# Performance work log

Measured on AMD Instinct MI355X. Metric: run time of the kernel, lower is better.

The kernel has to match this reference:

```python
import jax, jax.numpy as jnp
import numpy as np

TOP_K = 2


def setup_inputs() -> dict:
    key = jax.random.key(0)
    ks = jax.random.split(key, 6)
    B, S, H, I, E = 4, 2048, 1024, 4096, 8
    x = jax.random.normal(ks[0], (B, S, H), dtype=jnp.float32)
    Wr = jax.random.normal(ks[1], (H, E), dtype=jnp.float32) * (1.0 / np.sqrt(H))
    W1 = jax.random.normal(ks[2], (E, H, I), dtype=jnp.float32) * (1.0 / np.sqrt(H))
    b1 = jnp.zeros((E, I), dtype=jnp.float32)
    W2 = jax.random.normal(ks[3], (E, I, H), dtype=jnp.float32) * (1.0 / np.sqrt(I))
    b2 = jnp.zeros((E, H), dtype=jnp.float32)
    return {"x": x, "Wr": Wr, "W1": W1, "b1": b1, "W2": W2, "b2": b2}


def reference(x, Wr, W1, b1, W2, b2):
    B, S, H = x.shape
    E = Wr.shape[1]
    xf = x.reshape(-1, H)                              # [T, H], T = B*S
    logits = xf @ Wr                                   # [T, E]
    probs = jax.nn.softmax(logits, axis=-1)
    rw, sel = jax.lax.top_k(probs, TOP_K)              # [T, K]
    rw = rw / jnp.sum(rw, axis=-1, keepdims=True)
    out = jnp.zeros_like(xf)
    # Loop over small fixed expert count; each token contributes only via its
    # top-k combine weight (zero weight == not routed, matching index_add).
    for i in range(E):
        wi = jnp.sum(jnp.where(sel == i, rw, 0.0), axis=-1)    # [T]
        h = jax.nn.silu(xf @ W1[i] + b1[i])                    # [T, I]
        out = out + (h @ W2[i] + b2[i]) * wi[:, None]
    return out.reshape(B, S, H)
```

## Files before the change

kernel.cpp:

```cpp
#include <hip/hip_runtime.h>
#include <cstdint>
#include <cstddef>

#define TTOK 8192
#define HDIM 1024
#define IDIM 4096
#define NEXP 8
#define PMAX 18432
#define WS_NEED 302260352ULL

#define SLOT1 24576
#define SLOT2 16384

typedef __attribute__((ext_vector_type(8))) short bf16x8;
typedef __attribute__((ext_vector_type(4))) float f32x4;

#define AS3 __attribute__((address_space(3)))
#define AS1 __attribute__((address_space(1)))

__device__ __forceinline__ void gld16(const void* g, void* s) {
  __builtin_amdgcn_global_load_lds((const AS1 void*)g, (AS3 void*)s, 16, 0, 0);
}

__device__ __forceinline__ void pinned_barrier() {
  __builtin_amdgcn_sched_barrier(0);
  __builtin_amdgcn_s_barrier();
  __builtin_amdgcn_sched_barrier(0);
}

__device__ __forceinline__ unsigned short f2b(float f) {
  unsigned u = __builtin_bit_cast(unsigned, f);
  unsigned r = ((u >> 16) & 1u) + 0x7FFFu;
  return (unsigned short)((u + r) >> 16);
}

__device__ __forceinline__ float b2f(unsigned short u) {
  return __builtin_bit_cast(float, ((unsigned)u) << 16);
}


__device__ __forceinline__ void router_body(
    int bid, int t, const float* __restrict__ x, const float* __restrict__ wr,
    unsigned short* __restrict__ xb, int* __restrict__ t2e,
    float* __restrict__ t2w)
{
  const int tok = bid * 4 + (t >> 6);
  const int l = t & 63;
  const float* xr = x + (size_t)tok * HDIM;
  float acc[8] = {0.f,0.f,0.f,0.f,0.f,0.f,0.f,0.f};
  #pragma unroll
  for (int j = 0; j < 4; ++j) {
    const int base = j * 256 + l * 4;
    const float4 xv = *(const float4*)(xr + base);
    const float xa[4] = {xv.x, xv.y, xv.z, xv.w};
    ushort4 ub;
    ub.x = f2b(xa[0]); ub.y = f2b(xa[1]); ub.z = f2b(xa[2]); ub.w = f2b(xa[3]);
    *(ushort4*)(xb + (size_t)tok * HDIM + base) = ub;
    #pragma unroll
    for (int ii = 0; ii < 4; ++ii) {
      const float4 w0 = *(const float4*)(wr + (size_t)(base + ii) * 8);
      const float4 w1 = *(const float4*)(wr + (size_t)(base + ii) * 8 + 4);
      acc[0] += xa[ii] * w0.x; acc[1] += xa[ii] * w0.y;
      acc[2] += xa[ii] * w0.z; acc[3] += xa[ii] * w0.w;
      acc[4] += xa[ii] * w1.x; acc[5] += xa[ii] * w1.y;
      acc[6] += xa[ii] * w1.z; acc[7] += xa[ii] * w1.w;
    }
  }
  #pragma unroll
  for (int e = 0; e < 8; ++e) {
    float v = acc[e];
    #pragma unroll
    for (int off = 32; off > 0; off >>= 1) v += __shfl_xor(v, off);
    acc[e] = v;
  }
  if (l == 0) {
    float l0 = -1e30f; int i0 = 0;
    #pragma unroll
    for (int e = 0; e < 8; ++e) if (acc[e] > l0) { l0 = acc[e]; i0 = e; }
    float l1 = -1e30f; int i1 = (i0 == 0) ? 1 : 0;
    #pragma unroll
    for (int e = 0; e < 8; ++e) if (e != i0 && acc[e] > l1) { l1 = acc[e]; i1 = e; }
    const float w0 = 1.f / (1.f + expf(l1 - l0));
    t2e[tok * 2] = i0; t2e[tok * 2 + 1] = i1;
    t2w[tok * 2] = w0; t2w[tok * 2 + 1] = 1.f - w0;
  }
}

__device__ __forceinline__ void packT_body(
    int bid, int t, uint32_t* __restrict__ plds,
    const float* __restrict__ src, unsigned short* __restrict__ dst,
    int K, int N)
{
  const int tiles_n = N >> 8, tiles_k = K >> 5;
  const int e = bid / (tiles_k * tiles_n);
  const int rem = bid % (tiles_k * tiles_n);
  const int kt = rem / tiles_n, it = rem % tiles_n;
  const float* S = src + (size_t)e * K * N + (size_t)kt * 32 * N + (size_t)it * 256;
  unsigned short* D = dst + (size_t)e * N * K + (size_t)it * 256 * K + (size_t)kt * 32;
  #pragma unroll
  for (int q = 0; q < 4; ++q) {
    const int task = q * 256 + t;
    const int i4 = task & 63, kp = task >> 6;
    const float* p0 = S + (size_t)(2 * kp) * N + i4 * 4;
    const float4 r0 = *(const float4*)p0;
    const float4 r1 = *(const float4*)(p0 + N);
    const float a0[4] = {r0.x, r0.y, r0.z, r0.w};
    const float a1[4] = {r1.x, r1.y, r1.z, r1.w};
    #pragma unroll
    for (int j = 0; j < 4; ++j)
      plds[(i4 * 4 + j) * 17 + kp] = (uint32_t)f2b(a0[j]) | ((uint32_t)f2b(a1[j]) << 16);
  }
  __syncthreads();
  #pragma unroll
  for (int r = 0; r < 4; ++r) {
    const int idx = r * 256 + t;
    const int il = idx >> 2, q4 = idx & 3;
    uint4 o;
    o.x = plds[il * 17 + q4 * 4 + 0];
    o.y = plds[il * 17 + q4 * 4 + 1];
    o.z = plds[il * 17 + q4 * 4 + 2];
    o.w = plds[il * 17 + q4 * 4 + 3];
    *(uint4*)(D + (size_t)il * K + q4 * 8) = o;
  }
}

__global__ __launch_bounds__(256, 2) void prep_k(
    const float* __restrict__ x, const float* __restrict__ wr,
    unsigned short* __restrict__ xb, int* __restrict__ t2e,
    float* __restrict__ t2w,
    const float* __restrict__ w1, unsigned short* __restrict__ w1t,
    const float* __restrict__ w2, unsigned short* __restrict__ w2t)
{
  __shared__ uint32_t plds[256 * 17];
  const int bid = blockIdx.x, t = threadIdx.x;
  if (bid < 2048) {
    router_body(bid, t, x, wr, xb, t2e, t2w);
  } else if (bid < 2048 + 4096) {
    packT_body(bid - 2048, t, plds, w1, w1t, HDIM, IDIM);
  } else {
    packT_body(bid - 6144, t, plds, w2, w2t, IDIM, HDIM);
  }
}

__global__ void scatter_k(const int* __restrict__ t2e, int* __restrict__ meta,
                          int* __restrict__ ltok, int* __restrict__ t2p)
{
  const int e = blockIdx.x;
  const int t = threadIdx.x, w = t >> 6, l = t & 63;
  __shared__ int part[4][8];
  __shared__ int soff, scnt;
  {
    int cnt[8] = {0,0,0,0,0,0,0,0};
    for (int c = 0; c < 32; ++c) {
      const int tok = (w * 32 + c) * 64 + l;
      const int e0 = t2e[2 * tok], e1 = t2e[2 * tok + 1];
      #pragma unroll
      for (int i = 0; i < 8; ++i)
        cnt[i] += __popcll(__ballot(e0 == i)) + __popcll(__ballot(e1 == i));
    }
    if (l == 0) {
      #pragma unroll
      for (int i = 0; i < 8; ++i) part[w][i] = cnt[i];
    }
  }
  __syncthreads();
  if (t == 0) {
    int off = 0, mycnt = 0, tot = 0;
    #pragma unroll
    for (int i = 0; i < 8; ++i) {
      const int s = part[0][i] + part[1][i] + part[2][i] + part[3][i];
      const int pad = (s + 255) & ~255;
      if (i == e) mycnt = s;
      if (i < e) off += pad;
      tot += pad;
    }
    soff = off; scnt = mycnt;
    meta[16 + e] = off;
    if (e == 0) meta[24] = tot;
  }
  __syncthreads();
  const int off = soff, cnt = scnt;

  __shared__ int wsum[4];
  __shared__ int base;
  if (t == 0) base = 0;
  __syncthreads();
  const unsigned long long lt = (1ULL << l) - 1ULL;
  for (int c = 0; c < TTOK / 256; ++c) {
    const int tok = c * 256 + t;
    const bool m0 = (t2e[2 * tok] == e);
    const bool m1 = (t2e[2 * tok + 1] == e);
    const unsigned long long b0 = __ballot(m0);
    const unsigned long long b1 = __ballot(m1);
    const int n0 = __popcll(b0), n1 = __popcll(b1);
    const int r0 = __popcll(b0 & lt);
    const int r1 = n0 + __popcll(b1 & lt);
    if (l == 0) wsum[w] = n0 + n1;
    __syncthreads();
    int wb = base;
    #pragma unroll
    for (int i = 0; i < 4; ++i) if (i < w) wb += wsum[i];
    const int tot = wsum[0] + wsum[1] + wsum[2] + wsum[3];
    __syncthreads();
    if (t == 0) base += tot;
    if (m0) { const int p = off + wb + r0; ltok[p] = tok; t2p[2 * tok] = p; }
    if (m1) { const int p = off + wb + r1; ltok[p] = tok; t2p[2 * tok + 1] = p; }
    __syncthreads();
  }
  const int padded = (cnt + 255) & ~255;
  for (int i = cnt + t; i < padded; i += 256) ltok[off + i] = -1;
}


__global__ __launch_bounds__(512, 4) void gemm1_k(
    const unsigned short* __restrict__ xb, const unsigned short* __restrict__ w1t,
    const float* __restrict__ b1, const int* __restrict__ meta,
    const int* __restrict__ ltok, unsigned short* __restrict__ h)
{
  const int wg = blockIdx.x;
  const int id = (wg & 7) * (2304 / 8) + (wg >> 3);
  const int mt = id >> 5, nt = id & 31;
  if (mt * 256 >= meta[24]) return;
  int e = 0;
  #pragma unroll
  for (int i = 1; i < 8; ++i) if (meta[16 + i] <= mt * 256) e = i;

  extern __shared__ char lds[];
  const int t = threadIdx.x;
  const int w = t >> 6, l = t & 63;
  const int wn = w & 1, wm = w >> 1;

  const unsigned short* asrc;
  {
    const int G = t;
    const int line = G >> 3, q = (G & 7) ^ (line & 7);
    const int row = 2 * line + (q >> 2), g = q & 3;
    asrc = w1t + ((size_t)e * IDIM + nt * 128 + row) * HDIM + g * 8;
  }
  const unsigned short* bsrc[2];
  #pragma unroll
  for (int c = 0; c < 2; ++c) {
    const int G = c * 512 + t;
    const int line = G >> 3, q = (G & 7) ^ (line & 7);
    const int row = 2 * line + (q >> 2), g = q & 3;
    int tok = ltok[mt * 256 + row]; if (tok < 0) tok = 0;
    bsrc[c] = xb + (size_t)tok * HDIM + g * 8;
  }

  const int lr = l & 15, lg = l >> 4;
  f32x4 acc[4][4] = {};

  auto STAGE = [&](int kt) {
    char* sb = lds + (kt % 3) * SLOT1;
    const int ks = kt * 32;
    gld16(asrc + ks, sb + w * 1024);
    gld16(bsrc[0] + ks, sb + 8192 + w * 1024);
    gld16(bsrc[1] + ks, sb + 16384 + w * 1024);
  };

  STAGE(0); STAGE(1);
  const int NT = HDIM / 32;
  for (int kt = 0; kt < NT; ++kt) {
    if (kt + 1 < NT) {
      asm volatile("s_waitcnt vmcnt(3)" ::: "memory");
    } else {
      asm volatile("s_waitcnt vmcnt(0)" ::: "memory");
    }
    pinned_barrier();
    const char* sl = lds + (kt % 3) * SLOT1;
    bf16x8 af[4], bf[4];
    #pragma unroll
    for (int f = 0; f < 4; ++f) {
      const int rowA = wn * 64 + f * 16 + lr;
      const int lineA = rowA >> 1;
      const int pA = (((rowA & 1) << 2) + lg) ^ (lineA & 7);
      af[f] = *(const bf16x8*)(sl + lineA * 128 + pA * 16);
      const int rowB = wm * 64 + f * 16 + lr;
      const int lineB = rowB >> 1;
      const int pB = (((rowB & 1) << 2) + lg) ^ (lineB & 7);
      bf[f] = *(const bf16x8*)(sl + 8192 + lineB * 128 + pB * 16);
    }
    if (kt + 2 < NT) STAGE(kt + 2);
    __builtin_amdgcn_s_setprio(1);
    #pragma unroll
    for (int fm = 0; fm < 4; ++fm)
      #pragma unroll
      for (int fn = 0; fn < 4; ++fn)
        acc[fm][fn] = __builtin_amdgcn_mfma_f32_16x16x32_bf16(af[fm], bf[fn], acc[fm][fn], 0, 0, 0);
    __builtin_amdgcn_s_setprio(0);
    pinned_barrier();
  }

  const int lg4 = lg * 4;
  #pragma unroll
  for (int fm = 0; fm < 4; ++fm) {
    const int ib = nt * 128 + wn * 64 + fm * 16 + lg4;
    const float4 b1v = *(const float4*)(b1 + e * IDIM + ib);
    #pragma unroll
    for (int fn = 0; fn < 4; ++fn) {
      const int trow = mt * 256 + wm * 64 + fn * 16 + lr;
      const float v0 = acc[fm][fn][0] + b1v.x;
      const float v1 = acc[fm][fn][1] + b1v.y;
      const float v2 = acc[fm][fn][2] + b1v.z;
      const float v3 = acc[fm][fn][3] + b1v.w;
      ushort4 st;
      st.x = f2b(v0 / (1.f + __expf(-v0)));
      st.y = f2b(v1 / (1.f + __expf(-v1)));
      st.z = f2b(v2 / (1.f + __expf(-v2)));
      st.w = f2b(v3 / (1.f + __expf(-v3)));
      *(ushort4*)(h + (size_t)trow * IDIM + ib) = st;
    }
  }
}

__global__ __launch_bounds__(256, 3) void gemm2_k(
    const unsigned short* __restrict__ h, const unsigned short* __restrict__ w2t,
    const int* __restrict__ meta, unsigned short* __restrict__ y)
{
  const int wg = blockIdx.x;
  const int id = (wg & 7) * (2304 / 8) + (wg >> 3);
  const int nt = id & 7, kh = (id >> 3) & 1, mt = id >> 4;
  if (mt * 128 >= meta[24]) return;
  int e = 0;
  #pragma unroll
  for (int i = 1; i < 8; ++i) if (meta[16 + i] <= mt * 128) e = i;

  extern __shared__ char lds[];
  const int t = threadIdx.x;
  const int w = t >> 6, l = t & 63;
  const int wn = w & 1, wm = w >> 1;
  const int kbase = kh * (IDIM / 2);

  const unsigned short* asrc[2]; const unsigned short* bsrc[2];
  #pragma unroll
  for (int c = 0; c < 2; ++c) {
    const int G = c * 256 + t;
    const int line = G >> 3, q = (G & 7) ^ (line & 7);
    const int row = 2 * line + (q >> 2), g = q & 3;
    asrc[c] = w2t + ((size_t)e * HDIM + nt * 128 + row) * IDIM + kbase + g * 8;
    bsrc[c] = h + (size_t)(mt * 128 + row) * IDIM + kbase + g * 8;
  }

  const int lr = l & 15, lg = l >> 4;
  f32x4 acc[4][4] = {};

  auto STAGE = [&](int kt) {
    char* sb = lds + (kt % 3) * SLOT2;
    const int ks = kt * 32;
    gld16(asrc[0] + ks, sb + w * 1024);
    gld16(asrc[1] + ks, sb + 4096 + w * 1024);
    gld16(bsrc[0] + ks, sb + 8192 + w * 1024);
    gld16(bsrc[1] + ks, sb + 12288 + w * 1024);
  };

  STAGE(0); STAGE(1);
  const int NT = IDIM / 2 / 32;
  for (int kt = 0; kt < NT; ++kt) {
    if (kt + 1 < NT) {
      asm volatile("s_waitcnt vmcnt(4)" ::: "memory");
    } else {
      asm volatile("s_waitcnt vmcnt(0)" ::: "memory");
    }
    pinned_barrier();
    const char* sl = lds + (kt % 3) * SLOT2;
    bf16x8 af[4], bf[4];
    #pragma unroll
    for (int f = 0; f < 4; ++f) {
      const int rowA = wn * 64 + f * 16 + lr;
      const int lineA = rowA >> 1;
      const int pA = (((rowA & 1) << 2) + lg) ^ (lineA & 7);
      af[f] = *(const bf16x8*)(sl + lineA * 128 + pA * 16);
      const int rowB = wm * 64 + f * 16 + lr;
      const int lineB = rowB >> 1;
      const int pB = (((rowB & 1) << 2) + lg) ^ (lineB & 7);
      bf[f] = *(const bf16x8*)(sl + 8192 + lineB * 128 + pB * 16);
    }
    if (kt + 2 < NT) STAGE(kt + 2);
    __builtin_amdgcn_s_setprio(1);
    #pragma unroll
    for (int fm = 0; fm < 4; ++fm)
      #pragma unroll
      for (int fn = 0; fn < 4; ++fn)
        acc[fm][fn] = __builtin_amdgcn_mfma_f32_16x16x32_bf16(af[fm], bf[fn], acc[fm][fn], 0, 0, 0);
    __builtin_amdgcn_s_setprio(0);
    pinned_barrier();
  }

  unsigned short* yo = y + (size_t)kh * PMAX * HDIM;
  const int lg4 = lg * 4;
  #pragma unroll
  for (int fm = 0; fm < 4; ++fm) {
    const int colb = nt * 128 + wn * 64 + fm * 16 + lg4;
    #pragma unroll
    for (int fn = 0; fn < 4; ++fn) {
      const int row = mt * 128 + wm * 64 + fn * 16 + lr;
      ushort4 st;
      st.x = f2b(acc[fm][fn][0]); st.y = f2b(acc[fm][fn][1]);
      st.z = f2b(acc[fm][fn][2]); st.w = f2b(acc[fm][fn][3]);
      *(ushort4*)(yo + (size_t)row * HDIM + colb) = st;
    }
  }
}

__global__ __launch_bounds__(256, 4) void combine_k(
    const unsigned short* __restrict__ y, const float* __restrict__ b2,
    const int* __restrict__ t2e, const float* __restrict__ t2w,
    const int* __restrict__ t2p, float* __restrict__ out)
{
  const int t = blockIdx.x * 4 + (threadIdx.x >> 6);
  const int l = threadIdx.x & 63;
  const int e0 = t2e[t * 2], e1 = t2e[t * 2 + 1];
  const float w0 = t2w[t * 2], w1v = t2w[t * 2 + 1];
  const int p0 = t2p[t * 2], p1 = t2p[t * 2 + 1];
  const unsigned short* ya0 = y + (size_t)p0 * HDIM;
  const unsigned short* yb0 = y + (size_t)PMAX * HDIM + (size_t)p0 * HDIM;
  const unsigned short* ya1 = y + (size_t)p1 * HDIM;
  const unsigned short* yb1 = y + (size_t)PMAX * HDIM + (size_t)p1 * HDIM;
  const float* bb0 = b2 + e0 * HDIM;
  const float* bb1 = b2 + e1 * HDIM;
  float* o = out + (size_t)t * HDIM;
  #pragma unroll
  for (int j = 0; j < 4; ++j) {
    const int c = j * 256 + l * 4;
    const ushort4 a0 = *(const ushort4*)(ya0 + c);
    const ushort4 a1 = *(const ushort4*)(yb0 + c);
    const ushort4 b0v = *(const ushort4*)(ya1 + c);
    const ushort4 b1u = *(const ushort4*)(yb1 + c);
    const float4 c0 = *(const float4*)(bb0 + c);
    const float4 c1 = *(const float4*)(bb1 + c);
    float4 r;
    r.x = w0 * (b2f(a0.x) + b2f(a1.x) + c0.x) + w1v * (b2f(b0v.x) + b2f(b1u.x) + c1.x);
    r.y = w0 * (b2f(a0.y) + b2f(a1.y) + c0.y) + w1v * (b2f(b0v.y) + b2f(b1u.y) + c1.y);
    r.z = w0 * (b2f(a0.z) + b2f(a1.z) + c0.z) + w1v * (b2f(b0v.z) + b2f(b1u.z) + c1.z);
    r.w = w0 * (b2f(a0.w) + b2f(a1.w) + c0.w) + w1v * (b2f(b0v.w) + b2f(b1u.w) + c1.w);
    *(float4*)(o + c) = r;
  }
}

__global__ void sentinel_k(float* out) { out[0] = 1.0e6f; }

extern "C" void kernel_launch(void* const* d_in, const int* in_sizes, int n_in,
                              void* d_out, int out_size, void* d_ws, size_t ws_size,
                              hipStream_t stream)
{
  (void)in_sizes; (void)n_in; (void)out_size;
  const float* x  = (const float*)d_in[0];
  const float* wr = (const float*)d_in[1];
  const float* w1 = (const float*)d_in[2];
  const float* b1 = (const float*)d_in[3];
  const float* w2 = (const float*)d_in[4];
  const float* b2 = (const float*)d_in[5];
  float* out = (float*)d_out;
  char* ws = (char*)d_ws;

  if (ws_size < WS_NEED) { sentinel_k<<<1, 1, 0, stream>>>(out); return; }

  unsigned short* xb  = (unsigned short*)(ws);
  unsigned short* w1t = (unsigned short*)(ws + 16777216);
  unsigned short* w2t = (unsigned short*)(ws + 83886080);
  unsigned short* h   = (unsigned short*)(ws + 150994944);
  int*   t2e  = (int*)(ws + 301989888);
  float* t2w  = (float*)(ws + 302055424);
  int*   ltok = (int*)(ws + 302120960);
  int*   t2p  = (int*)(ws + 302194688);
  int*   meta = (int*)(ws + 302260224);
  unsigned short* y = (unsigned short*)(ws);

  hipFuncSetAttribute((const void*)gemm1_k, hipFuncAttributeMaxDynamicSharedMemorySize, 3 * SLOT1);
  hipFuncSetAttribute((const void*)gemm2_k, hipFuncAttributeMaxDynamicSharedMemorySize, 3 * SLOT2);

  prep_k<<<10240, 256, 0, stream>>>(x, wr, xb, t2e, t2w, w1, w1t, w2, w2t);
  scatter_k<<<NEXP, 256, 0, stream>>>(t2e, meta, ltok, t2p);

  gemm1_k<<<72 * 32, 512, 3 * SLOT1, stream>>>(xb, w1t, b1, meta, ltok, h);
  gemm2_k<<<144 * 8 * 2, 256, 3 * SLOT2, stream>>>(h, w2t, meta, y);
  combine_k<<<TTOK / 4, 256, 0, stream>>>(y, b2, t2e, t2w, t2p, out);
}
```

Before: 536.0 us.

## Enlarge gemm1 tile to 256x256 with 64-wide K and phased ping-pong pipeline

The first expert GEMM now uses 256x256 output tiles per workgroup, with each wave computing a 128x64 sub-tile over K steps of 64, and double-buffers 128KB of LDS. Global-to-LDS loads are split into quarter-stages interleaved with MFMA phases. This raises data reuse per byte loaded and cuts the number of workgroups. In exchange, occupancy drops to 2 blocks per CU with higher register pressure, and there are more barriers per iteration.

```diff
diff --git a/kernel.cpp b/kernel.cpp
--- a/kernel.cpp
+++ b/kernel.cpp
@@ -9,7 +9,6 @@
 #define PMAX 18432
 #define WS_NEED 302260352ULL
 
-#define SLOT1 24576
 #define SLOT2 16384
 
 typedef __attribute__((ext_vector_type(8))) short bf16x8;
@@ -25,6 +24,11 @@
 __device__ __forceinline__ void pinned_barrier() {
   __builtin_amdgcn_sched_barrier(0);
   __builtin_amdgcn_s_barrier();
+  __builtin_amdgcn_sched_barrier(0);
+}
+
+__device__ __forceinline__ void wait_lds() {
+  asm volatile("s_waitcnt lgkmcnt(0)" ::: "memory");
   __builtin_amdgcn_sched_barrier(0);
 }
 
@@ -211,15 +215,14 @@
   for (int i = cnt + t; i < padded; i += 256) ltok[off + i] = -1;
 }
 
-
-__global__ __launch_bounds__(512, 4) void gemm1_k(
+__global__ __launch_bounds__(512, 2) void gemm1_k(
     const unsigned short* __restrict__ xb, const unsigned short* __restrict__ w1t,
     const float* __restrict__ b1, const int* __restrict__ meta,
     const int* __restrict__ ltok, unsigned short* __restrict__ h)
 {
   const int wg = blockIdx.x;
-  const int id = (wg & 7) * (2304 / 8) + (wg >> 3);
-  const int mt = id >> 5, nt = id & 31;
+  const int id = (wg & 7) * (1152 / 8) + (wg >> 3);
+  const int mt = id >> 4, nt = id & 15;
   if (mt * 256 >= meta[24]) return;
   int e = 0;
   #pragma unroll
@@ -228,77 +231,226 @@
   extern __shared__ char lds[];
   const int t = threadIdx.x;
   const int w = t >> 6, l = t & 63;
-  const int wn = w & 1, wm = w >> 1;
-
-  const unsigned short* asrc;
-  {
-    const int G = t;
-    const int line = G >> 3, q = (G & 7) ^ (line & 7);
-    const int row = 2 * line + (q >> 2), g = q & 3;
-    asrc = w1t + ((size_t)e * IDIM + nt * 128 + row) * HDIM + g * 8;
-  }
-  const unsigned short* bsrc[2];
-  #pragma unroll
-  for (int c = 0; c < 2; ++c) {
-    const int G = c * 512 + t;
-    const int line = G >> 3, q = (G & 7) ^ (line & 7);
-    const int row = 2 * line + (q >> 2), g = q & 3;
-    int tok = ltok[mt * 256 + row]; if (tok < 0) tok = 0;
-    bsrc[c] = xb + (size_t)tok * HDIM + g * 8;
-  }
-
+  const int wm = w >> 2, wn = w & 3;
   const int lr = l & 15, lg = l >> 4;
-  f32x4 acc[4][4] = {};
-
-  auto STAGE = [&](int kt) {
-    char* sb = lds + (kt % 3) * SLOT1;
-    const int ks = kt * 32;
-    gld16(asrc + ks, sb + w * 1024);
-    gld16(bsrc[0] + ks, sb + 8192 + w * 1024);
-    gld16(bsrc[1] + ks, sb + 16384 + w * 1024);
+
+  const int srow = t >> 3;
+  const int sg = (t & 7) ^ (srow & 7);
+  const unsigned short* asrc[2][2];
+  const unsigned short* bsrc[2][2];
+  #pragma unroll
+  for (int hh = 0; hh < 2; ++hh)
+    #pragma unroll
+    for (int s = 0; s < 2; ++s) {
+      const int row = hh * 128 + s * 64 + srow;
+      asrc[hh][s] = w1t + ((size_t)e * IDIM + nt * 256 + row) * HDIM + sg * 8;
+      int tok = ltok[mt * 256 + row]; if (tok < 0) tok = 0;
+      bsrc[hh][s] = xb + (size_t)tok * HDIM + sg * 8;
+    }
+
+  auto STG = [&](int kt, int o, int hh) {
+    char* d = lds + (kt & 1) * 65536 + o * 32768 + hh * 16384 + w * 1024;
+    const int ks = kt * 64;
+    const unsigned short* s0 = o ? bsrc[hh][0] : asrc[hh][0];
+    const unsigned short* s1 = o ? bsrc[hh][1] : asrc[hh][1];
+    gld16(s0 + ks, d);
+    gld16(s1 + ks, d + 8192);
   };
 
-  STAGE(0); STAGE(1);
-  const int NT = HDIM / 32;
-  for (int kt = 0; kt < NT; ++kt) {
-    if (kt + 1 < NT) {
-      asm volatile("s_waitcnt vmcnt(3)" ::: "memory");
-    } else {
-      asm volatile("s_waitcnt vmcnt(0)" ::: "memory");
-    }
-    pinned_barrier();
-    const char* sl = lds + (kt % 3) * SLOT1;
-    bf16x8 af[4], bf[4];
-    #pragma unroll
-    for (int f = 0; f < 4; ++f) {
-      const int rowA = wn * 64 + f * 16 + lr;
-      const int lineA = rowA >> 1;
-      const int pA = (((rowA & 1) << 2) + lg) ^ (lineA & 7);
-      af[f] = *(const bf16x8*)(sl + lineA * 128 + pA * 16);
-      const int rowB = wm * 64 + f * 16 + lr;
-      const int lineB = rowB >> 1;
-      const int pB = (((rowB & 1) << 2) + lg) ^ (lineB & 7);
-      bf[f] = *(const bf16x8*)(sl + 8192 + lineB * 128 + pB * 16);
-    }
-    if (kt + 2 < NT) STAGE(kt + 2);
-    __builtin_amdgcn_s_setprio(1);
-    #pragma unroll
-    for (int fm = 0; fm < 4; ++fm)
-      #pragma unroll
-      for (int fn = 0; fn < 4; ++fn)
-        acc[fm][fn] = __builtin_amdgcn_mfma_f32_16x16x32_bf16(af[fm], bf[fn], acc[fm][fn], 0, 0, 0);
+  f32x4 acc[8][4] = {};
+  const int NITER = (HDIM / 64) / 2;
+
+  STG(0, 1, 0); STG(0, 1, 1);
+  STG(0, 0, 0); STG(0, 0, 1);
+  STG(1, 1, 0); STG(1, 1, 1);
+  asm volatile("s_waitcnt vmcnt(4)" ::: "memory");
+  pinned_barrier();
+
+  for (int it = 0; it < NITER; ++it) {
+    const int t1 = 2 * it + 1, t2 = 2 * it + 2, t3 = 2 * it + 3;
+    const bool pf = (it + 1 < NITER);
+    const char* sA0 = lds + wm * 16384;
+    const char* sB0 = lds + 32768 + (wn >> 1) * 16384;
+    const char* sA1 = sA0 + 65536;
+    const char* sB1 = sB0 + 65536;
+    const int rB = (wn & 1) * 64;
+
+    bf16x8 af[4][2], b01[2][2], b23[2][2];
+
+    #pragma unroll
+    for (int fm = 0; fm < 4; ++fm)
+      #pragma unroll
+      for (int ks = 0; ks < 2; ++ks) {
+        const int row = fm * 16 + lr;
+        af[fm][ks] = *(const bf16x8*)(sA0 + row * 128 + (((ks << 2) + lg) ^ (row & 7)) * 16);
+      }
+    #pragma unroll
+    for (int fn = 0; fn < 2; ++fn)
+      #pragma unroll
+      for (int ks = 0; ks < 2; ++ks) {
+        const int row = rB + fn * 16 + lr;
+        b01[fn][ks] = *(const bf16x8*)(sB0 + row * 128 + (((ks << 2) + lg) ^ (row & 7)) * 16);
+      }
+    STG(t1, 0, 0);
+    pinned_barrier(); wait_lds();
+    __builtin_amdgcn_s_setprio(1);
+    #pragma unroll
+    for (int fm = 0; fm < 4; ++fm)
+      #pragma unroll
+      for (int fn = 0; fn < 2; ++fn) {
+        acc[fm][fn] = __builtin_amdgcn_mfma_f32_16x16x32_bf16(af[fm][0], b01[fn][0], acc[fm][fn], 0, 0, 0);
+        acc[fm][fn] = __builtin_amdgcn_mfma_f32_16x16x32_bf16(af[fm][1], b01[fn][1], acc[fm][fn], 0, 0, 0);
+      }
+    __builtin_amdgcn_s_setprio(0);
+    pinned_barrier();
+
+    #pragma unroll
+    for (int fn = 0; fn < 2; ++fn)
+      #pragma unroll
+      for (int ks = 0; ks < 2; ++ks) {
+        const int row = rB + (fn + 2) * 16 + lr;
+        b23[fn][ks] = *(const bf16x8*)(sB0 + row * 128 + (((ks << 2) + lg) ^ (row & 7)) * 16);
+      }
+    STG(t1, 0, 1);
+    pinned_barrier(); wait_lds();
+    __builtin_amdgcn_s_setprio(1);
+    #pragma unroll
+    for (int fm = 0; fm < 4; ++fm)
+      #pragma unroll
+      for (int fn = 0; fn < 2; ++fn) {
+        acc[fm][fn + 2] = __builtin_amdgcn_mfma_f32_16x16x32_bf16(af[fm][0], b23[fn][0], acc[fm][fn + 2], 0, 0, 0);
+        acc[fm][fn + 2] = __builtin_amdgcn_mfma_f32_16x16x32_bf16(af[fm][1], b23[fn][1], acc[fm][fn + 2], 0, 0, 0);
+      }
+    __builtin_amdgcn_s_setprio(0);
+    pinned_barrier();
+
+    #pragma unroll
+    for (int fm = 0; fm < 4; ++fm)
+      #pragma unroll
+      for (int ks = 0; ks < 2; ++ks) {
+        const int row = (fm + 4) * 16 + lr;
+        af[fm][ks] = *(const bf16x8*)(sA0 + row * 128 + (((ks << 2) + lg) ^ (row & 7)) * 16);
+      }
+    if (pf) STG(t2, 1, 0);
+    pinned_barrier(); wait_lds();
+    __builtin_amdgcn_s_setprio(1);
+    #pragma unroll
+    for (int fm = 0; fm < 4; ++fm)
+      #pragma unroll
+      for (int fn = 0; fn < 2; ++fn) {
+        acc[fm + 4][fn] = __builtin_amdgcn_mfma_f32_16x16x32_bf16(af[fm][0], b01[fn][0], acc[fm + 4][fn], 0, 0, 0);
+        acc[fm + 4][fn] = __builtin_amdgcn_mfma_f32_16x16x32_bf16(af[fm][1], b01[fn][1], acc[fm + 4][fn], 0, 0, 0);
+      }
+    __builtin_amdgcn_s_setprio(0);
+    pinned_barrier();
+
+    if (pf) STG(t2, 1, 1);
+    if (pf) { asm volatile("s_waitcnt vmcnt(4)" ::: "memory"); }
+    else    { asm volatile("s_waitcnt vmcnt(0)" ::: "memory"); }
+    pinned_barrier();
+    __builtin_amdgcn_s_setprio(1);
+    #pragma unroll
+    for (int fm = 0; fm < 4; ++fm)
+      #pragma unroll
+      for (int fn = 0; fn < 2; ++fn) {
+        acc[fm + 4][fn + 2] = __builtin_amdgcn_mfma_f32_16x16x32_bf16(af[fm][0], b23[fn][0], acc[fm + 4][fn + 2], 0, 0, 0);
+        acc[fm + 4][fn + 2] = __builtin_amdgcn_mfma_f32_16x16x32_bf16(af[fm][1], b23[fn][1], acc[fm + 4][fn + 2], 0, 0, 0);
+      }
+    __builtin_amdgcn_s_setprio(0);
+    pinned_barrier();
+
+    #pragma unroll
+    for (int fm = 0; fm < 4; ++fm)
+      #pragma unroll
+      for (int ks = 0; ks < 2; ++ks) {
+        const int row = fm * 16 + lr;
+        af[fm][ks] = *(const bf16x8*)(sA1 + row * 128 + (((ks << 2) + lg) ^ (row & 7)) * 16);
+      }
+    #pragma unroll
+    for (int fn = 0; fn < 2; ++fn)
+      #pragma unroll
+      for (int ks = 0; ks < 2; ++ks) {
+        const int row = rB + fn * 16 + lr;
+        b01[fn][ks] = *(const bf16x8*)(sB1 + row * 128 + (((ks << 2) + lg) ^ (row & 7)) * 16);
+      }
+    if (pf) STG(t2, 0, 0);
+    pinned_barrier(); wait_lds();
+    __builtin_amdgcn_s_setprio(1);
+    #pragma unroll
+    for (int fm = 0; fm < 4; ++fm)
+      #pragma unroll
+      for (int fn = 0; fn < 2; ++fn) {
+        acc[fm][fn] = __builtin_amdgcn_mfma_f32_16x16x32_bf16(af[fm][0], b01[fn][0], acc[fm][fn], 0, 0, 0);
+        acc[fm][fn] = __builtin_amdgcn_mfma_f32_16x16x32_bf16(af[fm][1], b01[fn][1], acc[fm][fn], 0, 0, 0);
+      }
+    __builtin_amdgcn_s_setprio(0);
+    pinned_barrier();
+
+    #pragma unroll
+    for (int fn = 0; fn < 2; ++fn)
+      #pragma unroll
+      for (int ks = 0; ks < 2; ++ks) {
+        const int row = rB + (fn + 2) * 16 + lr;
+        b23[fn][ks] = *(const bf16x8*)(sB1 + row * 128 + (((ks << 2) + lg) ^ (row & 7)) * 16);
+      }
+    if (pf) STG(t2, 0, 1);
+    pinned_barrier(); wait_lds();
+    __builtin_amdgcn_s_setprio(1);
+    #pragma unroll
+    for (int fm = 0; fm < 4; ++fm)
+      #pragma unroll
+      for (int fn = 0; fn < 2; ++fn) {
+        acc[fm][fn + 2] = __builtin_amdgcn_mfma_f32_16x16x32_bf16(af[fm][0], b23[fn][0], acc[fm][fn + 2], 0, 0, 0);
+        acc[fm][fn + 2] = __builtin_amdgcn_mfma_f32_16x16x32_bf16(af[fm][1], b23[fn][1], acc[fm][fn + 2], 0, 0, 0);
+      }
+    __builtin_amdgcn_s_setprio(0);
+    pinned_barrier();
+
+    #pragma unroll
+    for (int fm = 0; fm < 4; ++fm)
+      #pragma unroll
+      for (int ks = 0; ks < 2; ++ks) {
+        const int row = (fm + 4) * 16 + lr;
+        af[fm][ks] = *(const bf16x8*)(sA1 + row * 128 + (((ks << 2) + lg) ^ (row & 7)) * 16);
+      }
+    if (pf) STG(t3, 1, 0);
+    pinned_barrier(); wait_lds();
+    __builtin_amdgcn_s_setprio(1);
+    #pragma unroll
+    for (int fm = 0; fm < 4; ++fm)
+      #pragma unroll
+      for (int fn = 0; fn < 2; ++fn) {
+        acc[fm + 4][fn] = __builtin_amdgcn_mfma_f32_16x16x32_bf16(af[fm][0], b01[fn][0], acc[fm + 4][fn], 0, 0, 0);
+        acc[fm + 4][fn] = __builtin_amdgcn_mfma_f32_16x16x32_bf16(af[fm][1], b01[fn][1], acc[fm + 4][fn], 0, 0, 0);
+      }
+    __builtin_amdgcn_s_setprio(0);
+    pinned_barrier();
+
+    if (pf) {
+      STG(t3, 1, 1);
+      asm volatile("s_waitcnt vmcnt(4)" ::: "memory");
+    }
+    pinned_barrier();
+    __builtin_amdgcn_s_setprio(1);
+    #pragma unroll
+    for (int fm = 0; fm < 4; ++fm)
+      #pragma unroll
+      for (int fn = 0; fn < 2; ++fn) {
+        acc[fm + 4][fn + 2] = __builtin_amdgcn_mfma_f32_16x16x32_bf16(af[fm][0], b23[fn][0], acc[fm + 4][fn + 2], 0, 0, 0);
+        acc[fm + 4][fn + 2] = __builtin_amdgcn_mfma_f32_16x16x32_bf16(af[fm][1], b23[fn][1], acc[fm + 4][fn + 2], 0, 0, 0);
+      }
     __builtin_amdgcn_s_setprio(0);
     pinned_barrier();
   }
 
   const int lg4 = lg * 4;
   #pragma unroll
-  for (int fm = 0; fm < 4; ++fm) {
-    const int ib = nt * 128 + wn * 64 + fm * 16 + lg4;
+  for (int fm = 0; fm < 8; ++fm) {
+    const int ib = nt * 256 + wm * 128 + fm * 16 + lg4;
     const float4 b1v = *(const float4*)(b1 + e * IDIM + ib);
     #pragma unroll
     for (int fn = 0; fn < 4; ++fn) {
-      const int trow = mt * 256 + wm * 64 + fn * 16 + lr;
+      const int trow = mt * 256 + wn * 64 + fn * 16 + lr;
       const float v0 = acc[fm][fn][0] + b1v.x;
       const float v1 = acc[fm][fn][1] + b1v.y;
       const float v2 = acc[fm][fn][2] + b1v.z;
@@ -466,13 +618,13 @@
   int*   meta = (int*)(ws + 302260224);
   unsigned short* y = (unsigned short*)(ws);
 
-  hipFuncSetAttribute((const void*)gemm1_k, hipFuncAttributeMaxDynamicSharedMemorySize, 3 * SLOT1);
+  hipFuncSetAttribute((const void*)gemm1_k, hipFuncAttributeMaxDynamicSharedMemorySize, 131072);
   hipFuncSetAttribute((const void*)gemm2_k, hipFuncAttributeMaxDynamicSharedMemorySize, 3 * SLOT2);
 
   prep_k<<<10240, 256, 0, stream>>>(x, wr, xb, t2e, t2w, w1, w1t, w2, w2t);
   scatter_k<<<NEXP, 256, 0, stream>>>(t2e, meta, ltok, t2p);
 
-  gemm1_k<<<72 * 32, 512, 3 * SLOT1, stream>>>(xb, w1t, b1, meta, ltok, h);
+  gemm1_k<<<72 * 16, 512, 131072, stream>>>(xb, w1t, b1, meta, ltok, h);
   gemm2_k<<<144 * 8 * 2, 256, 3 * SLOT2, stream>>>(h, w2t, meta, y);
   combine_k<<<TTOK / 4, 256, 0, stream>>>(y, b2, t2e, t2w, t2p, out);
 }
```

Result: faster. 520.5 us (-2.9%).

## Enlarge per-wave MFMA tiles to 256x128 in both expert GEMMs

Applied to the files above, without the earlier changes.

Both expert GEMMs now use 256-thread workgroups computing 256(N)x128(M) tiles, so each wave holds an 8x4 accumulator grid instead of 4x4. gemm1 moves from 512 threads with a 128x256 tile to 256 threads, and gemm2 doubles its N tile. The aim is more MFMA work per LDS fragment load and fewer workgroups re-reading weights, at the cost of higher register pressure and lower occupancy (launch bounds of 2). The barrier scheduling fences are also relaxed so the compiler can move some instructions across the loop-end barrier.

```diff
diff --git a/kernel.cpp b/kernel.cpp
--- a/kernel.cpp
+++ b/kernel.cpp
@@ -9,8 +9,7 @@
 #define PMAX 18432
 #define WS_NEED 302260352ULL
 
-#define SLOT1 24576
-#define SLOT2 16384
+#define SLOTG 24576
 
 typedef __attribute__((ext_vector_type(8))) short bf16x8;
 typedef __attribute__((ext_vector_type(4))) float f32x4;
@@ -22,10 +21,12 @@
   __builtin_amdgcn_global_load_lds((const AS1 void*)g, (AS3 void*)s, 16, 0, 0);
 }
 
-__device__ __forceinline__ void pinned_barrier() {
-  __builtin_amdgcn_sched_barrier(0);
+__device__ __forceinline__ void bar_fence() {
   __builtin_amdgcn_s_barrier();
-  __builtin_amdgcn_sched_barrier(0);
+  __builtin_amdgcn_sched_barrier(0xF);
+}
+__device__ __forceinline__ void bar_raw() {
+  __builtin_amdgcn_s_barrier();
 }
 
 __device__ __forceinline__ unsigned short f2b(float f) {
@@ -212,93 +213,98 @@
 }
 
 
-__global__ __launch_bounds__(512, 4) void gemm1_k(
+__global__ __launch_bounds__(256, 2) void gemm1_k(
     const unsigned short* __restrict__ xb, const unsigned short* __restrict__ w1t,
     const float* __restrict__ b1, const int* __restrict__ meta,
     const int* __restrict__ ltok, unsigned short* __restrict__ h)
 {
   const int wg = blockIdx.x;
   const int id = (wg & 7) * (2304 / 8) + (wg >> 3);
-  const int mt = id >> 5, nt = id & 31;
-  if (mt * 256 >= meta[24]) return;
+  const int mt = id >> 4, nt = id & 15;
+  if (mt * 128 >= meta[24]) return;
   int e = 0;
   #pragma unroll
-  for (int i = 1; i < 8; ++i) if (meta[16 + i] <= mt * 256) e = i;
+  for (int i = 1; i < 8; ++i) if (meta[16 + i] <= mt * 128) e = i;
 
   extern __shared__ char lds[];
   const int t = threadIdx.x;
   const int w = t >> 6, l = t & 63;
   const int wn = w & 1, wm = w >> 1;
-
-  const unsigned short* asrc;
-  {
-    const int G = t;
+  const int lr = l & 15, lg = l >> 4;
+
+  const unsigned short* asrc[4];
+  #pragma unroll
+  for (int c = 0; c < 4; ++c) {
+    const int G = c * 256 + t;
     const int line = G >> 3, q = (G & 7) ^ (line & 7);
     const int row = 2 * line + (q >> 2), g = q & 3;
-    asrc = w1t + ((size_t)e * IDIM + nt * 128 + row) * HDIM + g * 8;
+    asrc[c] = w1t + ((size_t)e * IDIM + nt * 256 + row) * HDIM + g * 8;
   }
   const unsigned short* bsrc[2];
   #pragma unroll
   for (int c = 0; c < 2; ++c) {
-    const int G = c * 512 + t;
+    const int G = c * 256 + t;
     const int line = G >> 3, q = (G & 7) ^ (line & 7);
     const int row = 2 * line + (q >> 2), g = q & 3;
-    int tok = ltok[mt * 256 + row]; if (tok < 0) tok = 0;
+    int tok = ltok[mt * 128 + row]; if (tok < 0) tok = 0;
     bsrc[c] = xb + (size_t)tok * HDIM + g * 8;
   }
 
-  const int lr = l & 15, lg = l >> 4;
-  f32x4 acc[4][4] = {};
+  f32x4 acc[8][4] = {};
 
   auto STAGE = [&](int kt) {
-    char* sb = lds + (kt % 3) * SLOT1;
+    char* sb = lds + (kt % 3) * SLOTG;
     const int ks = kt * 32;
-    gld16(asrc + ks, sb + w * 1024);
-    gld16(bsrc[0] + ks, sb + 8192 + w * 1024);
-    gld16(bsrc[1] + ks, sb + 16384 + w * 1024);
+    #pragma unroll
+    for (int c = 0; c < 4; ++c) gld16(asrc[c] + ks, sb + c * 4096 + w * 1024);
+    #pragma unroll
+    for (int c = 0; c < 2; ++c) gld16(bsrc[c] + ks, sb + 16384 + c * 4096 + w * 1024);
   };
 
   STAGE(0); STAGE(1);
   const int NT = HDIM / 32;
   for (int kt = 0; kt < NT; ++kt) {
     if (kt + 1 < NT) {
-      asm volatile("s_waitcnt vmcnt(3)" ::: "memory");
+      asm volatile("s_waitcnt vmcnt(6)" ::: "memory");
     } else {
       asm volatile("s_waitcnt vmcnt(0)" ::: "memory");
     }
-    pinned_barrier();
-    const char* sl = lds + (kt % 3) * SLOT1;
-    bf16x8 af[4], bf[4];
-    #pragma unroll
-    for (int f = 0; f < 4; ++f) {
-      const int rowA = wn * 64 + f * 16 + lr;
+    bar_fence();
+    const char* sl = lds + (kt % 3) * SLOTG;
+    bf16x8 af[8], bf[4];
+    #pragma unroll
+    for (int f = 0; f < 8; ++f) {
+      const int rowA = wn * 128 + f * 16 + lr;
       const int lineA = rowA >> 1;
       const int pA = (((rowA & 1) << 2) + lg) ^ (lineA & 7);
       af[f] = *(const bf16x8*)(sl + lineA * 128 + pA * 16);
+    }
+    #pragma unroll
+    for (int f = 0; f < 4; ++f) {
       const int rowB = wm * 64 + f * 16 + lr;
       const int lineB = rowB >> 1;
       const int pB = (((rowB & 1) << 2) + lg) ^ (lineB & 7);
-      bf[f] = *(const bf16x8*)(sl + 8192 + lineB * 128 + pB * 16);
+      bf[f] = *(const bf16x8*)(sl + 16384 + lineB * 128 + pB * 16);
     }
     if (kt + 2 < NT) STAGE(kt + 2);
     __builtin_amdgcn_s_setprio(1);
     #pragma unroll
-    for (int fm = 0; fm < 4; ++fm)
+    for (int fm = 0; fm < 8; ++fm)
       #pragma unroll
       for (int fn = 0; fn < 4; ++fn)
         acc[fm][fn] = __builtin_amdgcn_mfma_f32_16x16x32_bf16(af[fm], bf[fn], acc[fm][fn], 0, 0, 0);
     __builtin_amdgcn_s_setprio(0);
-    pinned_barrier();
+    bar_raw();
   }
 
   const int lg4 = lg * 4;
   #pragma unroll
-  for (int fm = 0; fm < 4; ++fm) {
-    const int ib = nt * 128 + wn * 64 + fm * 16 + lg4;
+  for (int fm = 0; fm < 8; ++fm) {
+    const int ib = nt * 256 + wn * 128 + fm * 16 + lg4;
     const float4 b1v = *(const float4*)(b1 + e * IDIM + ib);
     #pragma unroll
     for (int fn = 0; fn < 4; ++fn) {
-      const int trow = mt * 256 + wm * 64 + fn * 16 + lr;
+      const int trow = mt * 128 + wm * 64 + fn * 16 + lr;
       const float v0 = acc[fm][fn][0] + b1v.x;
       const float v1 = acc[fm][fn][1] + b1v.y;
       const float v2 = acc[fm][fn][2] + b1v.z;
@@ -313,13 +319,13 @@
   }
 }
 
-__global__ __launch_bounds__(256, 3) void gemm2_k(
+__global__ __launch_bounds__(256, 2) void gemm2_k(
     const unsigned short* __restrict__ h, const unsigned short* __restrict__ w2t,
     const int* __restrict__ meta, unsigned short* __restrict__ y)
 {
   const int wg = blockIdx.x;
-  const int id = (wg & 7) * (2304 / 8) + (wg >> 3);
-  const int nt = id & 7, kh = (id >> 3) & 1, mt = id >> 4;
+  const int id = (wg & 7) * (1152 / 8) + (wg >> 3);
+  const int nt = id & 3, kh = (id >> 2) & 1, mt = id >> 3;
   if (mt * 128 >= meta[24]) return;
   int e = 0;
   #pragma unroll
@@ -329,68 +335,78 @@
   const int t = threadIdx.x;
   const int w = t >> 6, l = t & 63;
   const int wn = w & 1, wm = w >> 1;
+  const int lr = l & 15, lg = l >> 4;
   const int kbase = kh * (IDIM / 2);
 
-  const unsigned short* asrc[2]; const unsigned short* bsrc[2];
+  const unsigned short* asrc[4];
+  #pragma unroll
+  for (int c = 0; c < 4; ++c) {
+    const int G = c * 256 + t;
+    const int line = G >> 3, q = (G & 7) ^ (line & 7);
+    const int row = 2 * line + (q >> 2), g = q & 3;
+    asrc[c] = w2t + ((size_t)e * HDIM + nt * 256 + row) * IDIM + kbase + g * 8;
+  }
+  const unsigned short* bsrc[2];
   #pragma unroll
   for (int c = 0; c < 2; ++c) {
     const int G = c * 256 + t;
     const int line = G >> 3, q = (G & 7) ^ (line & 7);
     const int row = 2 * line + (q >> 2), g = q & 3;
-    asrc[c] = w2t + ((size_t)e * HDIM + nt * 128 + row) * IDIM + kbase + g * 8;
     bsrc[c] = h + (size_t)(mt * 128 + row) * IDIM + kbase + g * 8;
   }
 
-  const int lr = l & 15, lg = l >> 4;
-  f32x4 acc[4][4] = {};
+  f32x4 acc[8][4] = {};
 
   auto STAGE = [&](int kt) {
-    char* sb = lds + (kt % 3) * SLOT2;
+    char* sb = lds + (kt % 3) * SLOTG;
     const int ks = kt * 32;
-    gld16(asrc[0] + ks, sb + w * 1024);
-    gld16(asrc[1] + ks, sb + 4096 + w * 1024);
-    gld16(bsrc[0] + ks, sb + 8192 + w * 1024);
-    gld16(bsrc[1] + ks, sb + 12288 + w * 1024);
+    #pragma unroll
+    for (int c = 0; c < 4; ++c) gld16(asrc[c] + ks, sb + c * 4096 + w * 1024);
+    #pragma unroll
+    for (int c = 0; c < 2; ++c) gld16(bsrc[c] + ks, sb + 16384 + c * 4096 + w * 1024);
   };
 
   STAGE(0); STAGE(1);
   const int NT = IDIM / 2 / 32;
   for (int kt = 0; kt < NT; ++kt) {
     if (kt + 1 < NT) {
-      asm volatile("s_waitcnt vmcnt(4)" ::: "memory");
+      asm volatile("s_waitcnt vmcnt(6)" ::: "memory");
     } else {
       asm volatile("s_waitcnt vmcnt(0)" ::: "memory");
     }
-    pinned_barrier();
-    const char* sl = lds + (kt % 3) * SLOT2;
-    bf16x8 af[4], bf[4];
-    #pragma unroll
-    for (int f = 0; f < 4; ++f) {
-      const int rowA = wn * 64 + f * 16 + lr;
+    bar_fence();
+    const char* sl = lds + (kt % 3) * SLOTG;
+    bf16x8 af[8], bf[4];
+    #pragma unroll
+    for (int f = 0; f < 8; ++f) {
+      const int rowA = wn * 128 + f * 16 + lr;
       const int lineA = rowA >> 1;
       const int pA = (((rowA & 1) << 2) + lg) ^ (lineA & 7);
       af[f] = *(const bf16x8*)(sl + lineA * 128 + pA * 16);
+    }
+    #pragma unroll
+    for (int f = 0; f < 4; ++f) {
       const int rowB = wm * 64 + f * 16 + lr;
       const int lineB = rowB >> 1;
       const int pB = (((rowB & 1) << 2) + lg) ^ (lineB & 7);
-      bf[f] = *(const bf16x8*)(sl + 8192 + lineB * 128 + pB * 16);
+      bf[f] = *(const bf16x8*)(sl + 16384 + lineB * 128 + pB * 16);
     }
     if (kt + 2 < NT) STAGE(kt + 2);
     __builtin_amdgcn_s_setprio(1);
     #pragma unroll
-    for (int fm = 0; fm < 4; ++fm)
+    for (int fm = 0; fm < 8; ++fm)
       #pragma unroll
       for (int fn = 0; fn < 4; ++fn)
         acc[fm][fn] = __builtin_amdgcn_mfma_f32_16x16x32_bf16(af[fm], bf[fn], acc[fm][fn], 0, 0, 0);
     __builtin_amdgcn_s_setprio(0);
-    pinned_barrier();
+    bar_raw();
   }
 
   unsigned short* yo = y + (size_t)kh * PMAX * HDIM;
   const int lg4 = lg * 4;
   #pragma unroll
-  for (int fm = 0; fm < 4; ++fm) {
-    const int colb = nt * 128 + wn * 64 + fm * 16 + lg4;
+  for (int fm = 0; fm < 8; ++fm) {
+    const int colb = nt * 256 + wn * 128 + fm * 16 + lg4;
     #pragma unroll
     for (int fn = 0; fn < 4; ++fn) {
       const int row = mt * 128 + wm * 64 + fn * 16 + lr;
@@ -466,13 +482,13 @@
   int*   meta = (int*)(ws + 302260224);
   unsigned short* y = (unsigned short*)(ws);
 
-  hipFuncSetAttribute((const void*)gemm1_k, hipFuncAttributeMaxDynamicSharedMemorySize, 3 * SLOT1);
-  hipFuncSetAttribute((const void*)gemm2_k, hipFuncAttributeMaxDynamicSharedMemorySize, 3 * SLOT2);
+  hipFuncSetAttribute((const void*)gemm1_k, hipFuncAttributeMaxDynamicSharedMemorySize, 3 * SLOTG);
+  hipFuncSetAttribute((const void*)gemm2_k, hipFuncAttributeMaxDynamicSharedMemorySize, 3 * SLOTG);
 
   prep_k<<<10240, 256, 0, stream>>>(x, wr, xb, t2e, t2w, w1, w1t, w2, w2t);
   scatter_k<<<NEXP, 256, 0, stream>>>(t2e, meta, ltok, t2p);
 
-  gemm1_k<<<72 * 32, 512, 3 * SLOT1, stream>>>(xb, w1t, b1, meta, ltok, h);
-  gemm2_k<<<144 * 8 * 2, 256, 3 * SLOT2, stream>>>(h, w2t, meta, y);
+  gemm1_k<<<144 * 16, 256, 3 * SLOTG, stream>>>(xb, w1t, b1, meta, ltok, h);
+  gemm2_k<<<144 * 4 * 2, 256, 3 * SLOTG, stream>>>(h, w2t, meta, y);
   combine_k<<<TTOK / 4, 256, 0, stream>>>(y, b2, t2e, t2w, t2p, out);
 }
```

Measured after the change: 501.1 us. 6.5% less time.
